# Kernel tuning notes

Measured on AMD Instinct MI355X. Metric: run time of the kernel, lower is better.

Reference implementation:

```python
import jax, jax.numpy as jnp
import numpy as np

N_TOKENS = 262144
N_EXPERTS = 256
TOP_K = 8


def setup_inputs() -> dict:
    key = jax.random.key(0)
    logits = jax.random.normal(key, (N_TOKENS, N_EXPERTS), dtype=jnp.float32)
    return {"logits": logits}


def reference(logits):
    # softmax gating in float32 (matches F.softmax(..., dtype=torch.float))
    routing_weights = jax.nn.softmax(logits.astype(jnp.float32), axis=1)
    # top-k selection over expert dim
    topk_weights, topk_ids = jax.lax.top_k(routing_weights, TOP_K)  # [N, K]
    # renormalize selected weights (norm_topk_prob=True)
    topk_weights = topk_weights / jnp.sum(topk_weights, axis=-1, keepdims=True)
    # histogram of expert ids, equivalent to torch.histc(bins=E, min=0, max=E)
    tokens_per_expert = jax.ops.segment_sum(
        jnp.ones_like(topk_ids.reshape(-1), dtype=jnp.float32),
        topk_ids.reshape(-1),
        num_segments=N_EXPERTS,
    )
    return logits, topk_weights, topk_ids, tokens_per_expert
```

## Files before the change

kernel.cpp:

```cpp
#include <hip/hip_runtime.h>
#include <math.h>


constexpr int NEXP   = 256;
constexpr int TOPK   = 8;
constexpr int TPB    = 256;
constexpr int WAVES  = TPB / 64;
constexpr int CHUNK  = 16;
constexpr int NCHUNK = NEXP / CHUNK;
constexpr int STRIDE = CHUNK + 1;
constexpr int F4T    = 4;

__global__ __launch_bounds__(TPB) void router_kernel(
    const float* __restrict__ logits,
    float* __restrict__ out_logits,
    float* __restrict__ out_w,
    float* __restrict__ out_id,
    float* __restrict__ counts)
{
    __shared__ float tile[WAVES][64 * STRIDE];
    __shared__ int   hist[NEXP];

    const int tid  = threadIdx.x;
    const int wave = tid >> 6;
    const int lane = tid & 63;
    const int tokw0 = blockIdx.x * TPB + wave * 64;

    hist[tid] = 0;
    __syncthreads();

    float v[TOPK];
    int   id[TOPK];
#pragma unroll
    for (int k = 0; k < TOPK; ++k) { v[k] = -INFINITY; id[k] = 0; }

    size_t gbase[F4T];
    int    lbase[F4T];
#pragma unroll
    for (int i = 0; i < F4T; ++i) {
        int f  = lane + 64 * i;
        int rr = f >> 2;
        int cc = f & 3;
        gbase[i] = (size_t)(tokw0 + rr) * NEXP + cc * 4;
        lbase[i] = rr * STRIDE + cc * 4;
    }

    float4 xA[F4T], xB[F4T];

#define STEP(C, XC, XN)                                                     \
    {                                                                       \
        const int c_ = (C);                                                 \
        if (c_ + 1 < NCHUNK) {                                              \
            const int off = (c_ + 1) * CHUNK;                               \
            _Pragma("unroll")                                               \
            for (int i = 0; i < F4T; ++i)                                   \
                XN[i] = *(const float4*)(logits + gbase[i] + off);          \
        }                                                                   \
        {                                                                   \
            const int off = c_ * CHUNK;                                     \
            _Pragma("unroll")                                               \
            for (int i = 0; i < F4T; ++i) {                                 \
                *(float4*)(out_logits + gbase[i] + off) = XC[i];            \
                float* t = &tile[wave][lbase[i]];                           \
                t[0] = XC[i].x; t[1] = XC[i].y;                             \
                t[2] = XC[i].z; t[3] = XC[i].w;                             \
            }                                                               \
        }                                                                   \
        const float* row = &tile[wave][lane * STRIDE];                      \
        const int c0 = c_ * CHUNK;                                          \
        _Pragma("unroll")                                                   \
        for (int j = 0; j < CHUNK; ++j) {                                   \
            float xx = row[j];                                              \
            int   xi = c0 + j;                                              \
            _Pragma("unroll")                                               \
            for (int k = 0; k < TOPK; ++k) {                                \
                bool  gt = xx > v[k];                                       \
                float tv = v[k];                                            \
                int   ti = id[k];                                           \
                v[k]  = gt ? xx : tv;                                       \
                id[k] = gt ? xi : ti;                                       \
                xx    = gt ? tv : xx;                                       \
                xi    = gt ? ti : xi;                                       \
            }                                                               \
        }                                                                   \
    }

#pragma unroll
    for (int i = 0; i < F4T; ++i)
        xA[i] = *(const float4*)(logits + gbase[i]);

#pragma unroll 1
    for (int c = 0; c < NCHUNK; c += 2) {
        STEP(c,     xA, xB);
        STEP(c + 1, xB, xA);
    }
#undef STEP

    float e[TOPK];
    float s = 0.f;
#pragma unroll
    for (int k = 0; k < TOPK; ++k) { e[k] = __expf(v[k] - v[0]); s += e[k]; }
    const float inv = 1.0f / s;

    const size_t token = (size_t)(tokw0 + lane);
    float4 w0 = make_float4(e[0] * inv, e[1] * inv, e[2] * inv, e[3] * inv);
    float4 w1 = make_float4(e[4] * inv, e[5] * inv, e[6] * inv, e[7] * inv);
    float4 i0 = make_float4((float)id[0], (float)id[1], (float)id[2], (float)id[3]);
    float4 i1 = make_float4((float)id[4], (float)id[5], (float)id[6], (float)id[7]);
    *(float4*)(out_w  + token * TOPK)     = w0;
    *(float4*)(out_w  + token * TOPK + 4) = w1;
    *(float4*)(out_id + token * TOPK)     = i0;
    *(float4*)(out_id + token * TOPK + 4) = i1;

#pragma unroll
    for (int k = 0; k < TOPK; ++k) atomicAdd(&hist[id[k]], 1);
    __syncthreads();
    atomicAdd(&counts[tid], (float)hist[tid]);
}

extern "C" void kernel_launch(void* const* d_in, const int* in_sizes, int n_in,
                              void* d_out, int out_size, void* d_ws, size_t ws_size,
                              hipStream_t stream) {
    const float* logits = (const float*)d_in[0];
    const int n_tokens  = in_sizes[0] / NEXP;

    float* out        = (float*)d_out;
    float* out_logits = out;
    float* out_w      = out_logits + (size_t)n_tokens * NEXP;
    float* out_id     = out_w      + (size_t)n_tokens * TOPK;
    float* counts     = out_id     + (size_t)n_tokens * TOPK;

    hipMemsetAsync(counts, 0, NEXP * sizeof(float), stream);

    const int blocks = n_tokens / TPB;
    router_kernel<<<blocks, TPB, 0, stream>>>(logits, out_logits, out_w,
                                              out_id, counts);
}
```

Measured before the change: 515.2 us.

## Split each token's top-k scan across two lanes and merge with bitonic network

Each token is now handled by two lanes in a wave, each scanning half of every 16-expert chunk. The two partial top-8 lists are merged with a cross-lane shuffle and a bitonic-style compare-exchange network, and each lane writes half of the outputs. Launch bounds gain an occupancy hint of 8 and the block count doubles. This shortens the serial per-thread insertion chain and raises parallelism. The cost is extra shuffles, merge work, and twice as many blocks each moving less data.

```diff
diff --git a/kernel.cpp b/kernel.cpp
--- a/kernel.cpp
+++ b/kernel.cpp
@@ -6,25 +6,30 @@
 constexpr int TOPK   = 8;
 constexpr int TPB    = 256;
 constexpr int WAVES  = TPB / 64;
+constexpr int TPW    = 32;
+constexpr int TPBLK  = WAVES * TPW;
 constexpr int CHUNK  = 16;
 constexpr int NCHUNK = NEXP / CHUNK;
+constexpr int HALF   = CHUNK / 2;
 constexpr int STRIDE = CHUNK + 1;
-constexpr int F4T    = 4;
+constexpr int F4T    = 2;
 
-__global__ __launch_bounds__(TPB) void router_kernel(
+__global__ __launch_bounds__(TPB, 8) void router_kernel(
     const float* __restrict__ logits,
     float* __restrict__ out_logits,
     float* __restrict__ out_w,
     float* __restrict__ out_id,
     float* __restrict__ counts)
 {
-    __shared__ float tile[WAVES][64 * STRIDE];
+    __shared__ float tile[WAVES][TPW * STRIDE];
     __shared__ int   hist[NEXP];
 
     const int tid  = threadIdx.x;
     const int wave = tid >> 6;
     const int lane = tid & 63;
-    const int tokw0 = blockIdx.x * TPB + wave * 64;
+    const int r    = lane & 31;
+    const int h    = lane >> 5;
+    const int tokw0 = blockIdx.x * TPBLK + wave * TPW;
 
     hist[tid] = 0;
     __syncthreads();
@@ -66,10 +71,10 @@
                 t[2] = XC[i].z; t[3] = XC[i].w;                             \
             }                                                               \
         }                                                                   \
-        const float* row = &tile[wave][lane * STRIDE];                      \
-        const int c0 = c_ * CHUNK;                                          \
+        const float* row = &tile[wave][r * STRIDE + h * HALF];              \
+        const int c0 = c_ * CHUNK + h * HALF;                               \
         _Pragma("unroll")                                                   \
-        for (int j = 0; j < CHUNK; ++j) {                                   \
+        for (int j = 0; j < HALF; ++j) {                                    \
             float xx = row[j];                                              \
             int   xi = c0 + j;                                              \
             _Pragma("unroll")                                               \
@@ -96,24 +101,49 @@
     }
 #undef STEP
 
+    float pv[TOPK]; int pid[TOPK];
+#pragma unroll
+    for (int k = 0; k < TOPK; ++k) {
+        pv[k]  = __shfl_xor(v[k],  32, 64);
+        pid[k] = __shfl_xor(id[k], 32, 64);
+    }
+    float mv[16]; int mi[16];
+#pragma unroll
+    for (int k = 0; k < TOPK; ++k) { mv[k] = v[k];      mi[k] = id[k]; }
+#pragma unroll
+    for (int k = 0; k < TOPK; ++k) { mv[8 + k] = pv[7 - k]; mi[8 + k] = pid[7 - k]; }
+
+#define CE(I, J)                                                            \
+    {                                                                       \
+        bool sw = (mv[J] > mv[I]) || ((mv[J] == mv[I]) && (mi[J] < mi[I])); \
+        float tv = mv[I]; int ti = mi[I];                                   \
+        mv[I] = sw ? mv[J] : mv[I];  mi[I] = sw ? mi[J] : mi[I];            \
+        mv[J] = sw ? tv : mv[J];     mi[J] = sw ? ti : mi[J];               \
+    }
+    CE(0, 8)  CE(1, 9)  CE(2, 10) CE(3, 11) CE(4, 12) CE(5, 13) CE(6, 14) CE(7, 15)
+    CE(0, 4)  CE(1, 5)  CE(2, 6)  CE(3, 7)
+    CE(0, 2)  CE(1, 3)  CE(4, 6)  CE(5, 7)
+    CE(0, 1)  CE(2, 3)  CE(4, 5)  CE(6, 7)
+#undef CE
+
     float e[TOPK];
     float s = 0.f;
 #pragma unroll
-    for (int k = 0; k < TOPK; ++k) { e[k] = __expf(v[k] - v[0]); s += e[k]; }
+    for (int k = 0; k < TOPK; ++k) { e[k] = __expf(mv[k] - mv[0]); s += e[k]; }
     const float inv = 1.0f / s;
 
-    const size_t token = (size_t)(tokw0 + lane);
-    float4 w0 = make_float4(e[0] * inv, e[1] * inv, e[2] * inv, e[3] * inv);
-    float4 w1 = make_float4(e[4] * inv, e[5] * inv, e[6] * inv, e[7] * inv);
-    float4 i0 = make_float4((float)id[0], (float)id[1], (float)id[2], (float)id[3]);
-    float4 i1 = make_float4((float)id[4], (float)id[5], (float)id[6], (float)id[7]);
-    *(float4*)(out_w  + token * TOPK)     = w0;
-    *(float4*)(out_w  + token * TOPK + 4) = w1;
-    *(float4*)(out_id + token * TOPK)     = i0;
-    *(float4*)(out_id + token * TOPK + 4) = i1;
+    const size_t token = (size_t)(tokw0 + r);
+    float4 wq, iq;
+    wq.x = (h ? e[4] : e[0]) * inv;  iq.x = (float)(h ? mi[4] : mi[0]);
+    wq.y = (h ? e[5] : e[1]) * inv;  iq.y = (float)(h ? mi[5] : mi[1]);
+    wq.z = (h ? e[6] : e[2]) * inv;  iq.z = (float)(h ? mi[6] : mi[2]);
+    wq.w = (h ? e[7] : e[3]) * inv;  iq.w = (float)(h ? mi[7] : mi[3]);
+    *(float4*)(out_w  + token * TOPK + h * 4) = wq;
+    *(float4*)(out_id + token * TOPK + h * 4) = iq;
 
 #pragma unroll
-    for (int k = 0; k < TOPK; ++k) atomicAdd(&hist[id[k]], 1);
+    for (int k = 0; k < 4; ++k)
+        atomicAdd(&hist[h ? mi[4 + k] : mi[k]], 1);
     __syncthreads();
     atomicAdd(&counts[tid], (float)hist[tid]);
 }
@@ -132,7 +162,7 @@
 
     hipMemsetAsync(counts, 0, NEXP * sizeof(float), stream);
 
-    const int blocks = n_tokens / TPB;
+    const int blocks = n_tokens / TPBLK;
     router_kernel<<<blocks, TPB, 0, stream>>>(logits, out_logits, out_w,
                                               out_id, counts);
 }
```

New measurement: 556.2 us. 8.0% more time.

## Split per-token top-k across 4 lanes with register lists and shuffle merge

Applied to the files above, without the earlier changes.

Removes the LDS transpose tile. Each lane now keeps four partial top-8 lists over its own quarter of the columns for four tokens, taken straight from the loaded float4s. The partial lists are merged across the 4 lanes with xor-shuffle bitonic merges, and each lane then writes two of the eight results. This drops LDS store/load traffic and barriers, but it quadruples the top-k register state and adds merge and shuffle work. A launch-bounds occupancy hint is also added, which may cause register spills.

```diff
diff --git a/kernel.cpp b/kernel.cpp
--- a/kernel.cpp
+++ b/kernel.cpp
@@ -5,45 +5,89 @@
 constexpr int NEXP   = 256;
 constexpr int TOPK   = 8;
 constexpr int TPB    = 256;
-constexpr int WAVES  = TPB / 64;
 constexpr int CHUNK  = 16;
 constexpr int NCHUNK = NEXP / CHUNK;
-constexpr int STRIDE = CHUNK + 1;
 constexpr int F4T    = 4;
 
-__global__ __launch_bounds__(TPB) void router_kernel(
+#define INS1(VL, IDL, xval, xidx)                                           \
+    {                                                                       \
+        float xx = (xval); int xi = (xidx);                                 \
+        _Pragma("unroll")                                                   \
+        for (int k = 0; k < TOPK; ++k) {                                    \
+            bool  gt = xx > VL[k];                                          \
+            float tv = VL[k];                                               \
+            int   ti = IDL[k];                                              \
+            VL[k]  = gt ? xx : tv;                                          \
+            IDL[k] = gt ? xi : ti;                                          \
+            xx     = gt ? tv : xx;                                          \
+            xi     = gt ? ti : xi;                                          \
+        }                                                                   \
+    }
+#define INS4(VL, IDL, Q, CB)                                                \
+    INS1(VL, IDL, (Q).x, (CB))     INS1(VL, IDL, (Q).y, (CB) + 1)           \
+    INS1(VL, IDL, (Q).z, (CB) + 2) INS1(VL, IDL, (Q).w, (CB) + 3)
+
+#define CE(I, J)                                                            \
+    {                                                                       \
+        bool sw = (mv[J] > mv[I]) || ((mv[J] == mv[I]) && (mi[J] < mi[I])); \
+        float tv = mv[I]; int ti = mi[I];                                   \
+        mv[I] = sw ? mv[J] : mv[I];  mi[I] = sw ? mi[J] : mi[I];            \
+        mv[J] = sw ? tv : mv[J];     mi[J] = sw ? ti : mi[J];               \
+    }
+
+#define MSTAGE(VL, IDL, XORW)                                               \
+    {                                                                       \
+        float pv[TOPK]; int pid[TOPK];                                      \
+        _Pragma("unroll")                                                   \
+        for (int k = 0; k < TOPK; ++k) {                                    \
+            pv[k]  = __shfl_xor(VL[k],  XORW, 64);                          \
+            pid[k] = __shfl_xor(IDL[k], XORW, 64);                          \
+        }                                                                   \
+        float mv[16]; int mi[16];                                           \
+        _Pragma("unroll")                                                   \
+        for (int k = 0; k < TOPK; ++k) {                                    \
+            mv[k] = VL[k];          mi[k] = IDL[k];                         \
+            mv[8 + k] = pv[7 - k];  mi[8 + k] = pid[7 - k];                 \
+        }                                                                   \
+        CE(0, 8) CE(1, 9) CE(2, 10) CE(3, 11)                               \
+        CE(4, 12) CE(5, 13) CE(6, 14) CE(7, 15)                             \
+        CE(0, 4) CE(1, 5) CE(2, 6) CE(3, 7)                                 \
+        CE(0, 2) CE(1, 3) CE(4, 6) CE(5, 7)                                 \
+        CE(0, 1) CE(2, 3) CE(4, 5) CE(6, 7)                                 \
+        _Pragma("unroll")                                                   \
+        for (int k = 0; k < TOPK; ++k) { VL[k] = mv[k]; IDL[k] = mi[k]; }   \
+    }
+
+__global__ __launch_bounds__(TPB, 4) void router_kernel(
     const float* __restrict__ logits,
     float* __restrict__ out_logits,
     float* __restrict__ out_w,
     float* __restrict__ out_id,
     float* __restrict__ counts)
 {
-    __shared__ float tile[WAVES][64 * STRIDE];
-    __shared__ int   hist[NEXP];
+    __shared__ int hist[NEXP];
 
     const int tid  = threadIdx.x;
     const int wave = tid >> 6;
     const int lane = tid & 63;
+    const int q    = lane & 3;
     const int tokw0 = blockIdx.x * TPB + wave * 64;
 
     hist[tid] = 0;
     __syncthreads();
 
-    float v[TOPK];
-    int   id[TOPK];
+    float v0[TOPK], v1[TOPK], v2[TOPK], v3[TOPK];
+    int  id0[TOPK], id1[TOPK], id2[TOPK], id3[TOPK];
 #pragma unroll
-    for (int k = 0; k < TOPK; ++k) { v[k] = -INFINITY; id[k] = 0; }
+    for (int k = 0; k < TOPK; ++k) {
+        v0[k] = v1[k] = v2[k] = v3[k] = -INFINITY;
+        id0[k] = id1[k] = id2[k] = id3[k] = 0;
+    }
 
     size_t gbase[F4T];
-    int    lbase[F4T];
 #pragma unroll
-    for (int i = 0; i < F4T; ++i) {
-        int f  = lane + 64 * i;
-        int rr = f >> 2;
-        int cc = f & 3;
-        gbase[i] = (size_t)(tokw0 + rr) * NEXP + cc * 4;
-        lbase[i] = rr * STRIDE + cc * 4;
-    }
+    for (int i = 0; i < F4T; ++i)
+        gbase[i] = (size_t)(tokw0 + (lane >> 2) + 16 * i) * NEXP + q * 4;
 
     float4 xA[F4T], xB[F4T];
 
@@ -59,30 +103,14 @@
         {                                                                   \
             const int off = c_ * CHUNK;                                     \
             _Pragma("unroll")                                               \
-            for (int i = 0; i < F4T; ++i) {                                 \
+            for (int i = 0; i < F4T; ++i)                                   \
                 *(float4*)(out_logits + gbase[i] + off) = XC[i];            \
-                float* t = &tile[wave][lbase[i]];                           \
-                t[0] = XC[i].x; t[1] = XC[i].y;                             \
-                t[2] = XC[i].z; t[3] = XC[i].w;                             \
-            }                                                               \
         }                                                                   \
-        const float* row = &tile[wave][lane * STRIDE];                      \
-        const int c0 = c_ * CHUNK;                                          \
-        _Pragma("unroll")                                                   \
-        for (int j = 0; j < CHUNK; ++j) {                                   \
-            float xx = row[j];                                              \
-            int   xi = c0 + j;                                              \
-            _Pragma("unroll")                                               \
-            for (int k = 0; k < TOPK; ++k) {                                \
-                bool  gt = xx > v[k];                                       \
-                float tv = v[k];                                            \
-                int   ti = id[k];                                           \
-                v[k]  = gt ? xx : tv;                                       \
-                id[k] = gt ? xi : ti;                                       \
-                xx    = gt ? tv : xx;                                       \
-                xi    = gt ? ti : xi;                                       \
-            }                                                               \
-        }                                                                   \
+        const int cb = c_ * CHUNK + q * 4;                                  \
+        INS4(v0, id0, XC[0], cb)                                            \
+        INS4(v1, id1, XC[1], cb)                                            \
+        INS4(v2, id2, XC[2], cb)                                            \
+        INS4(v3, id3, XC[3], cb)                                            \
     }
 
 #pragma unroll
@@ -96,24 +124,41 @@
     }
 #undef STEP
 
-    float e[TOPK];
-    float s = 0.f;
-#pragma unroll
-    for (int k = 0; k < TOPK; ++k) { e[k] = __expf(v[k] - v[0]); s += e[k]; }
-    const float inv = 1.0f / s;
+#define FINISH(VL, IDL, LIDX)                                               \
+    {                                                                       \
+        MSTAGE(VL, IDL, 1)                                                  \
+        MSTAGE(VL, IDL, 2)                                                  \
+            \
+        float e[TOPK]; float s = 0.f;                                       \
+        _Pragma("unroll")                                                   \
+        for (int k = 0; k < TOPK; ++k) {                                    \
+            e[k] = __expf(VL[k] - VL[0]); s += e[k];                        \
+        }                                                                   \
+        const float inv = 1.0f / s;                                         \
+        _Pragma("unroll")                                                   \
+        for (int k = 0; k < TOPK; ++k) e[k] *= inv;                         \
+             \
+        float wa = q == 0 ? e[0] : q == 1 ? e[2] : q == 2 ? e[4] : e[6];    \
+        float wb = q == 0 ? e[1] : q == 1 ? e[3] : q == 2 ? e[5] : e[7];    \
+        int   ia = q == 0 ? IDL[0] : q == 1 ? IDL[2]                        \
+                          : q == 2 ? IDL[4] : IDL[6];                       \
+        int   ib = q == 0 ? IDL[1] : q == 1 ? IDL[3]                        \
+                          : q == 2 ? IDL[5] : IDL[7];                       \
+        const size_t token = (size_t)(tokw0 + (lane >> 2) + 16 * (LIDX));   \
+        *(float2*)(out_w  + token * TOPK + q * 2) =                         \
+            make_float2(wa, wb);                                            \
+        *(float2*)(out_id + token * TOPK + q * 2) =                         \
+            make_float2((float)ia, (float)ib);                              \
+        atomicAdd(&hist[ia], 1);                                            \
+        atomicAdd(&hist[ib], 1);                                            \
+    }
 
-    const size_t token = (size_t)(tokw0 + lane);
-    float4 w0 = make_float4(e[0] * inv, e[1] * inv, e[2] * inv, e[3] * inv);
-    float4 w1 = make_float4(e[4] * inv, e[5] * inv, e[6] * inv, e[7] * inv);
-    float4 i0 = make_float4((float)id[0], (float)id[1], (float)id[2], (float)id[3]);
-    float4 i1 = make_float4((float)id[4], (float)id[5], (float)id[6], (float)id[7]);
-    *(float4*)(out_w  + token * TOPK)     = w0;
-    *(float4*)(out_w  + token * TOPK + 4) = w1;
-    *(float4*)(out_id + token * TOPK)     = i0;
-    *(float4*)(out_id + token * TOPK + 4) = i1;
+    FINISH(v0, id0, 0)
+    FINISH(v1, id1, 1)
+    FINISH(v2, id2, 2)
+    FINISH(v3, id3, 3)
+#undef FINISH
 
-#pragma unroll
-    for (int k = 0; k < TOPK; ++k) atomicAdd(&hist[id[k]], 1);
     __syncthreads();
     atomicAdd(&counts[tid], (float)hist[tid]);
 }
```

Measured after the change: 626.6 us. 21.6% more time.
